# Kernel optimization log

Hardware: AMD Instinct MI355X
Metric: run time of the kernel (lower is better)

## Reference

```python
import jax, jax.numpy as jnp
import numpy as np

DIM = 1024
HEADS = 16
HEAD_DIM = DIM // HEADS
WINDOW = 128


def setup_inputs() -> dict:
    key = jax.random.key(0)
    k1, k2, k3, k4 = jax.random.split(key, 4)
    B, T = 2, 2048
    x = jax.random.normal(k1, (B, T, DIM), dtype=jnp.float32)
    # nn.Linear(dim, 3*dim, bias=False): weight [3*dim, dim]; y = x @ W.T
    W_qkv = jax.random.normal(k2, (3 * DIM, DIM), dtype=jnp.float32) * (1.0 / np.sqrt(DIM))
    W_proj = jax.random.normal(k3, (DIM, DIM), dtype=jnp.float32) * (1.0 / np.sqrt(DIM))
    b_proj = jax.random.normal(k4, (DIM,), dtype=jnp.float32) * 0.01
    return {"x": x, "W_qkv": W_qkv, "W_proj": W_proj, "b_proj": b_proj}


def reference(x, W_qkv, W_proj, b_proj) -> jnp.ndarray:
    B, T, C = x.shape
    scale = HEAD_DIM ** -0.5
    qkv = jnp.einsum('btc,oc->bto', x, W_qkv)  # [B,T,3*D]
    qkv = qkv.reshape(B, T, 3, HEADS, HEAD_DIM)
    qkv = jnp.transpose(qkv, (2, 0, 3, 1, 4))  # [3,B,H,T,hd]
    q, k, v = qkv[0], qkv[1], qkv[2]
    # sliding-window mask: attend iff |i-j| <= WINDOW
    idx = jnp.arange(T)
    mask = jnp.abs(idx[:, None] - idx[None, :]) <= WINDOW  # [T,T]
    scores = jnp.einsum('bhqd,bhkd->bhqk', q, k) * scale  # [B,H,T,T]
    scores = jnp.where(mask[None, None], scores, jnp.finfo(scores.dtype).min)
    attn = jax.nn.softmax(scores, axis=-1)
    out = jnp.einsum('bhqk,bhkd->bhqd', attn, v)  # [B,H,T,hd]
    out = jnp.transpose(out, (0, 2, 1, 3)).reshape(B, T, C)
    return jnp.einsum('btc,oc->bto', out, W_proj) + b_proj
```

## Files before the change

### kernel.cpp

```cpp
#include <hip/hip_runtime.h>
#include <hip/hip_bf16.h>
#include <cstdint>
#include <cstddef>

#define DIMC 1024
#define HEADS 16
#define HD 64
#define WINDOW 128
#define BB 2
#define TT 2048
#define NTOK (BB*TT)
#define QKVN (3*DIMC)

typedef __bf16 bf16;
typedef __bf16 bf16x8 __attribute__((ext_vector_type(8)));
typedef __bf16 bf16x4 __attribute__((ext_vector_type(4)));
typedef float f32x4 __attribute__((ext_vector_type(4)));
typedef unsigned int u32;

typedef const __attribute__((address_space(1))) u32* gp1_t;
typedef __attribute__((address_space(3))) u32* lp3_t;

__device__ __forceinline__ void gload16(const void* g, void* l) {
  __builtin_amdgcn_global_load_lds((gp1_t)g, (lp3_t)l, 16, 0, 0);
}

__device__ __forceinline__ u32 lds_u32(const void* p) {
  return (u32)(uintptr_t)(__attribute__((address_space(3))) const void*)p;
}

__device__ __forceinline__ void BAR() {
  asm volatile("" ::: "memory");
  __builtin_amdgcn_s_barrier();
  asm volatile("" ::: "memory");
}

__global__ void cast3_kernel(const float* __restrict__ x,
                             const float* __restrict__ wq,
                             const float* __restrict__ wp,
                             bf16* __restrict__ xo,
                             bf16* __restrict__ wqo,
                             bf16* __restrict__ wpo) {
  const int NX = NTOK * DIMC / 4;
  const int NQ = QKVN * DIMC / 4;
  const int NP = DIMC * DIMC / 4;
  const int total = NX + NQ + NP;
  typedef float float4v __attribute__((ext_vector_type(4)));
  for (int i = blockIdx.x * blockDim.x + threadIdx.x; i < total;
       i += gridDim.x * blockDim.x) {
    const float4v* src; bf16* dst; int j;
    if (i < NX)            { src = (const float4v*)x;  dst = xo;  j = i; }
    else if (i < NX + NQ)  { src = (const float4v*)wq; dst = wqo; j = i - NX; }
    else                   { src = (const float4v*)wp; dst = wpo; j = i - NX - NQ; }
    float4v v = src[j];
    bf16x4 o;
    o[0] = (bf16)v[0]; o[1] = (bf16)v[1]; o[2] = (bf16)v[2]; o[3] = (bf16)v[3];
    ((bf16x4*)dst)[j] = o;
  }
}

__device__ __forceinline__ bf16x8 lds_frag(const bf16* base, int row, int colb) {
  const char* p = (const char*)base + row * 128 + (colb ^ ((row & 7) << 4));
  return *(const bf16x8*)p;
}

__global__ __launch_bounds__(512, 2) void gemm256_qkv_kernel(
    const bf16* __restrict__ A, const bf16* __restrict__ Bw,
    bf16* __restrict__ C) {
  constexpr int K = 1024;
  constexpr int NT = K / 64;
  __shared__ bf16 Alds[2][256 * 64];
  __shared__ bf16 Blds[2][192 * 64];

  const int tid = threadIdx.x;
  const int wid = tid >> 6, l = tid & 63;
  const int wm = wid >> 2, wn = wid & 3;
  const int lr = l & 15, lg = l >> 4;
  const int w8 = wid * 8;

  const int bid = blockIdx.x;
  const int wg = (bid & 7) * 32 + (bid >> 3);
  const int bm = wg & 15;
  const int bn = wg >> 4;

  const char* Ag = (const char*)A + (size_t)(bm * 256) * 2048;
  const char* Bg = (const char*)Bw + (size_t)(bn * 192) * 2048;

  auto stageA = [&](bf16* lds, int kt, int half) {
#pragma unroll
    for (int i = 0; i < 2; i++) {
      const int R0 = half * 64 + i * 128 + w8;
      const int r = R0 + (l >> 3);
      const char* src = Ag + (size_t)r * 2048 + kt * 128
                        + (((l & 7) * 16) ^ ((r & 7) << 4));
      gload16(src, lds + R0 * 64);
    }
  };
  auto stageB = [&](bf16* lds, int kt, int third) {
    const int R0 = third * 64 + w8;
    const int r = R0 + (l >> 3);
    const char* src = Bg + (size_t)r * 2048 + kt * 128
                      + (((l & 7) * 16) ^ ((r & 7) << 4));
    gload16(src, lds + R0 * 64);
  };

  stageB(Blds[0], 0, 0); stageB(Blds[0], 0, 1); stageB(Blds[0], 0, 2);
  stageA(Alds[0], 0, 0); stageA(Alds[0], 0, 1);
  stageB(Blds[1], 1, 0); stageB(Blds[1], 1, 1); stageB(Blds[1], 1, 2);
  stageA(Alds[1], 1, 0);
  asm volatile("s_waitcnt vmcnt(5)" ::: "memory");
  BAR();

  f32x4 acc[8][3] = {};

  auto ktile = [&](int kt, const bf16* Acur, const bf16* Bcur,
                   bf16* Anext, bf16* Acur_w, bf16* Bcur_w) {
    bf16x8 bfr[3][2];
#pragma unroll
    for (int mq = 0; mq < 4; ++mq) {
      bf16x8 afr[2][2];
      if (mq == 0) {
#pragma unroll
        for (int n = 0; n < 3; n++)
#pragma unroll
          for (int kk = 0; kk < 2; kk++)
            bfr[n][kk] = lds_frag(Bcur, wn * 48 + n * 16 + lr, kk * 64 + lg * 16);
      }
#pragma unroll
      for (int mi = 0; mi < 2; mi++)
#pragma unroll
        for (int kk = 0; kk < 2; kk++)
          afr[mi][kk] = lds_frag(Acur, wm * 128 + (2 * mq + mi) * 16 + lr,
                                 kk * 64 + lg * 16);
      if (mq == 0)      { if (kt + 1 < NT) stageA(Anext,  kt + 1, 1); }
      else if (mq == 1) { if (kt + 2 < NT) stageB(Bcur_w, kt + 2, 0); }
      else if (mq == 2) { if (kt + 2 < NT) { stageB(Bcur_w, kt + 2, 1);
                                             stageB(Bcur_w, kt + 2, 2); } }
      else              { if (kt + 2 < NT) stageA(Acur_w, kt + 2, 0); }
      BAR();
      asm volatile("s_waitcnt lgkmcnt(0)" ::: "memory");
      __builtin_amdgcn_s_setprio(1);
#pragma unroll
      for (int kk = 0; kk < 2; kk++)
#pragma unroll
        for (int mi = 0; mi < 2; mi++)
#pragma unroll
          for (int n = 0; n < 3; n++)
            acc[2 * mq + mi][n] = __builtin_amdgcn_mfma_f32_16x16x32_bf16(
                afr[mi][kk], bfr[n][kk], acc[2 * mq + mi][n], 0, 0, 0);
      __builtin_amdgcn_s_setprio(0);
      if (mq == 3) {
        if (kt >= NT - 2) asm volatile("s_waitcnt vmcnt(0)" ::: "memory");
        else              asm volatile("s_waitcnt vmcnt(5)" ::: "memory");
      }
      BAR();
    }
  };

  for (int kt2 = 0; kt2 < NT; kt2 += 2) {
    ktile(kt2,     Alds[0], Blds[0], Alds[1], Alds[0], Blds[0]);
    ktile(kt2 + 1, Alds[1], Blds[1], Alds[0], Alds[1], Blds[1]);
  }

#pragma unroll
  for (int m = 0; m < 8; m++) {
    const int row = bm * 256 + wm * 128 + m * 16 + lg * 4;
#pragma unroll
    for (int n = 0; n < 3; n++) {
      const int col = bn * 192 + wn * 48 + n * 16 + lr;
#pragma unroll
      for (int j = 0; j < 4; j++)
        C[(size_t)(row + j) * QKVN + col] = (bf16)acc[m][n][j];
    }
  }
}

template<int N_>
__global__ __launch_bounds__(256, 2) void gemm_bt_kernel(
    const bf16* __restrict__ A, const bf16* __restrict__ Bw,
    float* __restrict__ Cf, const float* __restrict__ bias) {
  constexpr int K = 1024;
  constexpr int KB = K * 2;
  __shared__ bf16 As[2][128 * 32];
  __shared__ bf16 Bs[2][128 * 32];

  const int tid = threadIdx.x;
  const int w = tid >> 6, l = tid & 63;
  const int bm = blockIdx.x & 31;
  const int bn = blockIdx.x >> 5;
  const int wm = w >> 1, wn = w & 1;
  const int lr = l & 15, lg = l >> 4;

  const int srow = w * 32 + (l >> 2);
  const int scolb = (l & 3) * 16;
  const char* Agb = (const char*)A + (size_t)(bm * 128 + srow) * KB + scolb;
  const char* Bgb = (const char*)Bw + (size_t)(bn * 128 + srow) * KB + scolb;

  f32x4 acc[4][4] = {};

  auto stage = [&](int buf, int t) {
    const char* ag = Agb + t * 64;
    const char* bg = Bgb + t * 64;
    gload16(ag,            &As[buf][(w * 32) * 32]);
    gload16(ag + 16 * KB,  &As[buf][(w * 32 + 16) * 32]);
    gload16(bg,            &Bs[buf][(w * 32) * 32]);
    gload16(bg + 16 * KB,  &Bs[buf][(w * 32 + 16) * 32]);
  };

  stage(0, 0);
  __syncthreads();
  constexpr int NTiles = K / 32;
  int buf = 0;
  for (int t = 0; t < NTiles; ++t) {
    if (t + 1 < NTiles) stage(buf ^ 1, t + 1);
    bf16x8 af[4], bfr[4];
#pragma unroll
    for (int m = 0; m < 4; m++)
      af[m] = *(const bf16x8*)&As[buf][(wm * 64 + m * 16 + lr) * 32 + lg * 8];
#pragma unroll
    for (int n = 0; n < 4; n++)
      bfr[n] = *(const bf16x8*)&Bs[buf][(wn * 64 + n * 16 + lr) * 32 + lg * 8];
#pragma unroll
    for (int m = 0; m < 4; m++)
#pragma unroll
      for (int n = 0; n < 4; n++)
        acc[m][n] = __builtin_amdgcn_mfma_f32_16x16x32_bf16(af[m], bfr[n], acc[m][n], 0, 0, 0);
    __syncthreads();
    buf ^= 1;
  }

#pragma unroll
  for (int m = 0; m < 4; m++) {
    const int row = bm * 128 + wm * 64 + m * 16 + lg * 4;
#pragma unroll
    for (int n = 0; n < 4; n++) {
      const int col = bn * 128 + wn * 64 + n * 16 + lr;
#pragma unroll
      for (int j = 0; j < 4; j++)
        Cf[(size_t)(row + j) * N_ + col] = acc[m][n][j] + bias[col];
    }
  }
}

__global__ __launch_bounds__(256, 4) void attn_kernel(const bf16* __restrict__ qkv,
                                                      bf16* __restrict__ out) {
  __shared__ bf16 Kl[2][64 * 64];
  __shared__ bf16 Vl[2][64 * 64];

  const int tid = threadIdx.x, w = tid >> 6, l = tid & 63;
  const int qb = blockIdx.x & 31, bh = blockIdx.x >> 5;
  const int b = bh >> 4, h = bh & 15;
  const int q0 = qb * 64;
  const int lr = l & 15, lg = l >> 4;
  const float SC = 0.18033688011f;

  const char* qkv_b = (const char*)qkv + (size_t)(b * TT) * (QKVN * 2);

  size_t koff[2]; u32 kdst[2];
#pragma unroll
  for (int i = 0; i < 2; i++) {
    const int R0 = 8 * (w + 4 * i);
    const int r = R0 + (l >> 3);
    const int colb = (((l & 7) * 16) ^ (((l >> 3) & 7) << 4));
    koff[i] = (size_t)r * (QKVN * 2) + (DIMC + h * HD) * 2 + colb;
    kdst[i] = (u32)(R0 * 64);
  }
  size_t voff[2]; u32 vdst[2];
#pragma unroll
  for (int i = 0; i < 2; i++) {
    const int c = tid + 256 * i;
    const int t = c >> 3, w_ = c & 7;
    const int kv = (t & 15) * 4 + (w_ >> 1);
    const int d  = (t >> 4) * 16 + (w_ & 1) * 8;
    voff[i] = (size_t)kv * (QKVN * 2) + (2 * DIMC + h * HD + d) * 2;
    vdst[i] = (u32)((w + 4 * i) * 512);
  }

  auto stage = [&](int buf, int kb) {
    const char* rowb = qkv_b + (size_t)(kb * 64) * (QKVN * 2);
#pragma unroll
    for (int i = 0; i < 2; i++)
      gload16(rowb + koff[i], &Kl[buf][kdst[i]]);
#pragma unroll
    for (int i = 0; i < 2; i++)
      gload16(rowb + voff[i], &Vl[buf][vdst[i]]);
  };

  bf16x8 qf[2];
  {
    const bf16* qp = qkv + (size_t)(b * TT + q0 + w * 16 + lr) * QKVN + h * HD + lg * 8;
    qf[0] = *(const bf16x8*)qp;
    qf[1] = *(const bf16x8*)(qp + 32);
  }

  f32x4 Oa[4] = {};
  float mrow = -1e30f, lrow = 0.f;

  int kb0 = qb - 2; if (kb0 < 0) kb0 = 0;
  int kb1 = qb + 2; if (kb1 > 31) kb1 = 31;

  stage(0, kb0);
  asm volatile("s_waitcnt vmcnt(0)" ::: "memory");
  BAR();

  for (int kb = kb0; kb <= kb1; ++kb) {
    const int c = (kb - kb0) & 1;
    if (kb + 1 <= kb1) stage(c ^ 1, kb + 1);

    const bf16* Kb = &Kl[c][0];
    f32x4 Sa[4] = {};
#pragma unroll
    for (int kf = 0; kf < 2; kf++)
#pragma unroll
      for (int nf = 0; nf < 4; nf++) {
        const char* kp = (const char*)Kb + (nf * 16 + lr) * 128
                         + ((kf * 64 + lg * 16) ^ ((lr & 7) << 4));
        bf16x8 kfr = *(const bf16x8*)kp;
        Sa[nf] = __builtin_amdgcn_mfma_f32_16x16x32_bf16(kfr, qf[kf], Sa[nf], 0, 0, 0);
      }

    bf16x4 tr0[4][2], tr1[4][2];
    {
      const u32 vbase = lds_u32(&Vl[c][0]) + l * 8;
#pragma unroll
      for (int nf = 0; nf < 4; nf++)
#pragma unroll
        for (int kf = 0; kf < 2; kf++) {
          const u32 a = vbase + (u32)((nf * 16 + kf * 8) * 128);
          asm volatile("ds_read_b64_tr_b16 %0, %1"
                       : "=v"(tr0[nf][kf]) : "v"(a));
          asm volatile("ds_read_b64_tr_b16 %0, %1 offset:512"
                       : "=v"(tr1[nf][kf]) : "v"(a));
        }
    }

    const int qrow = q0 + w * 16 + lr;
    const int kvb = kb * 64;
    float p[4][4];
    float mblk = -1e30f;
#pragma unroll
    for (int nf = 0; nf < 4; nf++)
#pragma unroll
      for (int j = 0; j < 4; j++) {
        int kv = kvb + nf * 16 + lg * 4 + j;
        int dq = qrow - kv;
        float s = Sa[nf][j] * SC;
        if (dq > WINDOW || dq < -WINDOW) s = -1e30f;
        p[nf][j] = s;
        mblk = fmaxf(mblk, s);
      }
    mblk = fmaxf(mblk, __shfl_xor(mblk, 16));
    mblk = fmaxf(mblk, __shfl_xor(mblk, 32));

    float mn = fmaxf(mrow, mblk);
    float scl = exp2f(mrow - mn);
    mrow = mn;

    float rsum = 0.f;
#pragma unroll
    for (int nf = 0; nf < 4; nf++)
#pragma unroll
      for (int j = 0; j < 4; j++) {
        float e = exp2f(p[nf][j] - mn);
        p[nf][j] = e;
        rsum += e;
      }
    rsum += __shfl_xor(rsum, 16);
    rsum += __shfl_xor(rsum, 32);
    lrow = lrow * scl + rsum;

    bf16x8 pa[2];
#pragma unroll
    for (int kf = 0; kf < 2; kf++)
#pragma unroll
      for (int e = 0; e < 4; e++) {
        pa[kf][e]     = (bf16)p[2 * kf][e];
        pa[kf][e + 4] = (bf16)p[2 * kf + 1][e];
      }

#pragma unroll
    for (int j = 0; j < 4; j++) {
      float so = __shfl(scl, lg * 4 + j);
#pragma unroll
      for (int nf = 0; nf < 4; nf++) Oa[nf][j] *= so;
    }

    asm volatile("s_waitcnt lgkmcnt(0)" ::: "memory");
    __builtin_amdgcn_sched_barrier(0);
#pragma unroll
    for (int nf = 0; nf < 4; nf++)
#pragma unroll
      for (int kf = 0; kf < 2; kf++) {
        bf16x8 vb;
#pragma unroll
        for (int e = 0; e < 4; e++) {
          vb[e]     = tr0[nf][kf][e];
          vb[e + 4] = tr1[nf][kf][e];
        }
        Oa[nf] = __builtin_amdgcn_mfma_f32_16x16x32_bf16(pa[kf], vb, Oa[nf], 0, 0, 0);
      }

    asm volatile("s_waitcnt vmcnt(0)" ::: "memory");
    BAR();
  }

  float lo[4];
#pragma unroll
  for (int j = 0; j < 4; j++) lo[j] = __shfl(lrow, lg * 4 + j);
#pragma unroll
  for (int nf = 0; nf < 4; nf++) {
#pragma unroll
    for (int j = 0; j < 4; j++) {
      int q = q0 + w * 16 + lg * 4 + j;
      int d = nf * 16 + lr;
      out[(size_t)(b * TT + q) * DIMC + h * HD + d] = (bf16)(Oa[nf][j] / lo[j]);
    }
  }
}

extern "C" void kernel_launch(void* const* d_in, const int* in_sizes, int n_in,
                              void* d_out, int out_size, void* d_ws, size_t ws_size,
                              hipStream_t stream) {
  const float* x     = (const float*)d_in[0];
  const float* Wqkv  = (const float*)d_in[1];
  const float* Wproj = (const float*)d_in[2];
  const float* bproj = (const float*)d_in[3];
  float* out = (float*)d_out;

  char* ws = (char*)d_ws;
  bf16* xb   = (bf16*)(ws);
  bf16* wqb  = (bf16*)(ws + 8388608);
  bf16* wpb  = (bf16*)(ws + 14680064);
  bf16* qkvb = (bf16*)(ws + 16777216);
  bf16* aob  = (bf16*)(ws + 41943040);

  cast3_kernel<<<2048, 256, 0, stream>>>(x, Wqkv, Wproj, xb, wqb, wpb);
  gemm256_qkv_kernel<<<256, 512, 0, stream>>>(xb, wqb, qkvb);
  attn_kernel<<<1024, 256, 0, stream>>>(qkvb, aob);
  gemm_bt_kernel<DIMC><<<dim3(32 * 8), 256, 0, stream>>>(aob, wpb, out, bproj);
}
```

Baseline: 89.44 us.

## Unify QKV and output projections into one 128x128 swizzled double-buffered GEMM

Replaces the 256x192 QKV GEMM (512 threads) and the simpler 128x128 K=32 projection GEMM with one templated 128x128 tile kernel. It uses K=64 XOR-swizzled LDS tiles, a two-stage global_load_lds prefetch, and an XCD-aware block remap. The QKV launch grows from 256 to 768 blocks to fill more CUs, at the cost of lower per-block data reuse than the larger tile. The output projection gains the swizzled, deeper-K pipelined loop.

```diff
diff --git a/kernel.cpp b/kernel.cpp
--- a/kernel.cpp
+++ b/kernel.cpp
@@ -64,169 +64,87 @@
   return *(const bf16x8*)p;
 }
 
-__global__ __launch_bounds__(512, 2) void gemm256_qkv_kernel(
+template<int N_, bool BF16OUT>
+__global__ __launch_bounds__(256, 2) void gemm128_kernel(
     const bf16* __restrict__ A, const bf16* __restrict__ Bw,
-    bf16* __restrict__ C) {
+    bf16* __restrict__ Cb, float* __restrict__ Cf,
+    const float* __restrict__ bias) {
   constexpr int K = 1024;
   constexpr int NT = K / 64;
-  __shared__ bf16 Alds[2][256 * 64];
-  __shared__ bf16 Blds[2][192 * 64];
+  __shared__ bf16 Al[2][128 * 64];
+  __shared__ bf16 Bl[2][128 * 64];
 
   const int tid = threadIdx.x;
-  const int wid = tid >> 6, l = tid & 63;
-  const int wm = wid >> 2, wn = wid & 3;
+  const int w = tid >> 6, l = tid & 63;
+  const int wm = w >> 1, wn = w & 1;
   const int lr = l & 15, lg = l >> 4;
-  const int w8 = wid * 8;
-
+
+  const int nwg = gridDim.x;
   const int bid = blockIdx.x;
-  const int wg = (bid & 7) * 32 + (bid >> 3);
-  const int bm = wg & 15;
-  const int bn = wg >> 4;
-
-  const char* Ag = (const char*)A + (size_t)(bm * 256) * 2048;
-  const char* Bg = (const char*)Bw + (size_t)(bn * 192) * 2048;
-
-  auto stageA = [&](bf16* lds, int kt, int half) {
-#pragma unroll
-    for (int i = 0; i < 2; i++) {
-      const int R0 = half * 64 + i * 128 + w8;
+  const int wg = (bid & 7) * (nwg >> 3) + (bid >> 3);
+  const int bm = wg & 31;
+  const int bn = wg >> 5;
+
+  const char* Ag = (const char*)A + (size_t)(bm * 128) * 2048;
+  const char* Bg = (const char*)Bw + (size_t)(bn * 128) * 2048;
+
+  auto stageT = [&](bf16* lds, const char* gbase, int kt) {
+#pragma unroll
+    for (int i = 0; i < 4; i++) {
+      const int R0 = w * 32 + i * 8;
       const int r = R0 + (l >> 3);
-      const char* src = Ag + (size_t)r * 2048 + kt * 128
+      const char* src = gbase + (size_t)r * 2048 + kt * 128
                         + (((l & 7) * 16) ^ ((r & 7) << 4));
       gload16(src, lds + R0 * 64);
     }
   };
-  auto stageB = [&](bf16* lds, int kt, int third) {
-    const int R0 = third * 64 + w8;
-    const int r = R0 + (l >> 3);
-    const char* src = Bg + (size_t)r * 2048 + kt * 128
-                      + (((l & 7) * 16) ^ ((r & 7) << 4));
-    gload16(src, lds + R0 * 64);
-  };
-
-  stageB(Blds[0], 0, 0); stageB(Blds[0], 0, 1); stageB(Blds[0], 0, 2);
-  stageA(Alds[0], 0, 0); stageA(Alds[0], 0, 1);
-  stageB(Blds[1], 1, 0); stageB(Blds[1], 1, 1); stageB(Blds[1], 1, 2);
-  stageA(Alds[1], 1, 0);
-  asm volatile("s_waitcnt vmcnt(5)" ::: "memory");
+
+  stageT(Al[0], Ag, 0); stageT(Bl[0], Bg, 0);
+  stageT(Al[1], Ag, 1); stageT(Bl[1], Bg, 1);
+  asm volatile("s_waitcnt vmcnt(8)" ::: "memory");
   BAR();
 
-  f32x4 acc[8][3] = {};
-
-  auto ktile = [&](int kt, const bf16* Acur, const bf16* Bcur,
-                   bf16* Anext, bf16* Acur_w, bf16* Bcur_w) {
-    bf16x8 bfr[3][2];
-#pragma unroll
-    for (int mq = 0; mq < 4; ++mq) {
-      bf16x8 afr[2][2];
-      if (mq == 0) {
-#pragma unroll
-        for (int n = 0; n < 3; n++)
-#pragma unroll
-          for (int kk = 0; kk < 2; kk++)
-            bfr[n][kk] = lds_frag(Bcur, wn * 48 + n * 16 + lr, kk * 64 + lg * 16);
-      }
-#pragma unroll
-      for (int mi = 0; mi < 2; mi++)
-#pragma unroll
-        for (int kk = 0; kk < 2; kk++)
-          afr[mi][kk] = lds_frag(Acur, wm * 128 + (2 * mq + mi) * 16 + lr,
-                                 kk * 64 + lg * 16);
-      if (mq == 0)      { if (kt + 1 < NT) stageA(Anext,  kt + 1, 1); }
-      else if (mq == 1) { if (kt + 2 < NT) stageB(Bcur_w, kt + 2, 0); }
-      else if (mq == 2) { if (kt + 2 < NT) { stageB(Bcur_w, kt + 2, 1);
-                                             stageB(Bcur_w, kt + 2, 2); } }
-      else              { if (kt + 2 < NT) stageA(Acur_w, kt + 2, 0); }
-      BAR();
-      asm volatile("s_waitcnt lgkmcnt(0)" ::: "memory");
-      __builtin_amdgcn_s_setprio(1);
+  f32x4 acc[4][4] = {};
+
+  for (int kt = 0; kt < NT; ++kt) {
+    const bf16* Ac = Al[kt & 1];
+    const bf16* Bc = Bl[kt & 1];
+
+    bf16x8 af[4][2], bf[4][2];
+#pragma unroll
+    for (int m = 0; m < 4; m++)
 #pragma unroll
       for (int kk = 0; kk < 2; kk++)
-#pragma unroll
-        for (int mi = 0; mi < 2; mi++)
-#pragma unroll
-          for (int n = 0; n < 3; n++)
-            acc[2 * mq + mi][n] = __builtin_amdgcn_mfma_f32_16x16x32_bf16(
-                afr[mi][kk], bfr[n][kk], acc[2 * mq + mi][n], 0, 0, 0);
-      __builtin_amdgcn_s_setprio(0);
-      if (mq == 3) {
-        if (kt >= NT - 2) asm volatile("s_waitcnt vmcnt(0)" ::: "memory");
-        else              asm volatile("s_waitcnt vmcnt(5)" ::: "memory");
-      }
-      BAR();
-    }
-  };
-
-  for (int kt2 = 0; kt2 < NT; kt2 += 2) {
-    ktile(kt2,     Alds[0], Blds[0], Alds[1], Alds[0], Blds[0]);
-    ktile(kt2 + 1, Alds[1], Blds[1], Alds[0], Alds[1], Blds[1]);
-  }
-
-#pragma unroll
-  for (int m = 0; m < 8; m++) {
-    const int row = bm * 256 + wm * 128 + m * 16 + lg * 4;
-#pragma unroll
-    for (int n = 0; n < 3; n++) {
-      const int col = bn * 192 + wn * 48 + n * 16 + lr;
-#pragma unroll
-      for (int j = 0; j < 4; j++)
-        C[(size_t)(row + j) * QKVN + col] = (bf16)acc[m][n][j];
-    }
-  }
-}
-
-template<int N_>
-__global__ __launch_bounds__(256, 2) void gemm_bt_kernel(
-    const bf16* __restrict__ A, const bf16* __restrict__ Bw,
-    float* __restrict__ Cf, const float* __restrict__ bias) {
-  constexpr int K = 1024;
-  constexpr int KB = K * 2;
-  __shared__ bf16 As[2][128 * 32];
-  __shared__ bf16 Bs[2][128 * 32];
-
-  const int tid = threadIdx.x;
-  const int w = tid >> 6, l = tid & 63;
-  const int bm = blockIdx.x & 31;
-  const int bn = blockIdx.x >> 5;
-  const int wm = w >> 1, wn = w & 1;
-  const int lr = l & 15, lg = l >> 4;
-
-  const int srow = w * 32 + (l >> 2);
-  const int scolb = (l & 3) * 16;
-  const char* Agb = (const char*)A + (size_t)(bm * 128 + srow) * KB + scolb;
-  const char* Bgb = (const char*)Bw + (size_t)(bn * 128 + srow) * KB + scolb;
-
-  f32x4 acc[4][4] = {};
-
-  auto stage = [&](int buf, int t) {
-    const char* ag = Agb + t * 64;
-    const char* bg = Bgb + t * 64;
-    gload16(ag,            &As[buf][(w * 32) * 32]);
-    gload16(ag + 16 * KB,  &As[buf][(w * 32 + 16) * 32]);
-    gload16(bg,            &Bs[buf][(w * 32) * 32]);
-    gload16(bg + 16 * KB,  &Bs[buf][(w * 32 + 16) * 32]);
-  };
-
-  stage(0, 0);
-  __syncthreads();
-  constexpr int NTiles = K / 32;
-  int buf = 0;
-  for (int t = 0; t < NTiles; ++t) {
-    if (t + 1 < NTiles) stage(buf ^ 1, t + 1);
-    bf16x8 af[4], bfr[4];
-#pragma unroll
-    for (int m = 0; m < 4; m++)
-      af[m] = *(const bf16x8*)&As[buf][(wm * 64 + m * 16 + lr) * 32 + lg * 8];
+        af[m][kk] = lds_frag(Ac, wm * 64 + m * 16 + lr, kk * 64 + lg * 16);
 #pragma unroll
     for (int n = 0; n < 4; n++)
-      bfr[n] = *(const bf16x8*)&Bs[buf][(wn * 64 + n * 16 + lr) * 32 + lg * 8];
-#pragma unroll
-    for (int m = 0; m < 4; m++)
-#pragma unroll
-      for (int n = 0; n < 4; n++)
-        acc[m][n] = __builtin_amdgcn_mfma_f32_16x16x32_bf16(af[m], bfr[n], acc[m][n], 0, 0, 0);
-    __syncthreads();
-    buf ^= 1;
+#pragma unroll
+      for (int kk = 0; kk < 2; kk++)
+        bf[n][kk] = lds_frag(Bc, wn * 64 + n * 16 + lr, kk * 64 + lg * 16);
+
+    asm volatile("s_waitcnt lgkmcnt(0)" ::: "memory");
+    __builtin_amdgcn_sched_barrier(0);
+    BAR();
+
+    if (kt + 2 < NT) {
+      stageT(Al[kt & 1], Ag, kt + 2);
+      stageT(Bl[kt & 1], Bg, kt + 2);
+    }
+
+    __builtin_amdgcn_s_setprio(1);
+#pragma unroll
+    for (int kk = 0; kk < 2; kk++)
+#pragma unroll
+      for (int m = 0; m < 4; m++)
+#pragma unroll
+        for (int n = 0; n < 4; n++)
+          acc[m][n] = __builtin_amdgcn_mfma_f32_16x16x32_bf16(
+              af[m][kk], bf[n][kk], acc[m][n], 0, 0, 0);
+    __builtin_amdgcn_s_setprio(0);
+
+    if (kt < NT - 2) asm volatile("s_waitcnt vmcnt(8)" ::: "memory");
+    else             asm volatile("s_waitcnt vmcnt(0)" ::: "memory");
+    BAR();
   }
 
 #pragma unroll
@@ -236,8 +154,12 @@
     for (int n = 0; n < 4; n++) {
       const int col = bn * 128 + wn * 64 + n * 16 + lr;
 #pragma unroll
-      for (int j = 0; j < 4; j++)
-        Cf[(size_t)(row + j) * N_ + col] = acc[m][n][j] + bias[col];
+      for (int j = 0; j < 4; j++) {
+        if constexpr (BF16OUT)
+          Cb[(size_t)(row + j) * N_ + col] = (bf16)acc[m][n][j];
+        else
+          Cf[(size_t)(row + j) * N_ + col] = acc[m][n][j] + bias[col];
+      }
     }
   }
 }
@@ -435,7 +357,7 @@
   bf16* aob  = (bf16*)(ws + 41943040);
 
   cast3_kernel<<<2048, 256, 0, stream>>>(x, Wqkv, Wproj, xb, wqb, wpb);
-  gemm256_qkv_kernel<<<256, 512, 0, stream>>>(xb, wqb, qkvb);
+  gemm128_kernel<QKVN, true><<<768, 256, 0, stream>>>(xb, wqb, qkvb, nullptr, nullptr);
   attn_kernel<<<1024, 256, 0, stream>>>(qkvb, aob);
-  gemm_bt_kernel<DIMC><<<dim3(32 * 8), 256, 0, stream>>>(aob, wpb, out, bproj);
-}
+  gemm128_kernel<DIMC, false><<<256, 256, 0, stream>>>(aob, wpb, nullptr, out, bproj);
+}
```

Result: no change. 90.22 us (+0.9%).
